# Kernel tuning notes

Measured on AMD Instinct MI355X. Metric: run time of the kernel, lower is better.

Reference implementation:

```python
import jax, jax.numpy as jnp
import numpy as np

PI = 3.141592653589793
DIM = 512          # entity/relation dim
HID = 2048         # MLP hidden dim
NREL = 500         # number of relations
NBASE = 30         # number of relation bases
B = 1024           # batch
EMB_RANGE = 0.0275 # (gamma+eps)/dim, ConE convention
AXIS_SCALE = 1.0
ARG_SCALE = 1.0
LN_EPS = 1e-5


def _ln(x):
    # LayerNorm, elementwise_affine=False
    m = x.mean(-1, keepdims=True)
    v = ((x - m) ** 2).mean(-1, keepdims=True)
    return (x - m) / jnp.sqrt(v + LN_EPS)


def _to_axis(x):
    return jnp.tanh(x) * PI


def _to_arg(x):
    return jnp.tanh(2 * x) * (PI / 2) + PI / 2


def _angle_scale(x, scale):
    return x / EMB_RANGE * scale


def setup_inputs() -> dict:
    key = jax.random.key(0)
    ks = jax.random.split(key, 16)
    D2 = 2 * DIM
    inp = {
        "source_embedding_axis": jax.random.normal(ks[0], (B, DIM), jnp.float32),
        "source_embedding_arg": jax.random.normal(ks[1], (B, DIM), jnp.float32),
        "rel_indices": jax.random.randint(ks[2], (B,), 0, NREL, jnp.int64)
        if jax.config.jax_enable_x64
        else jax.random.randint(ks[2], (B,), 0, NREL, jnp.int32),
        # rtrans branch params
        "rel_base": jax.random.normal(ks[3], (NBASE, D2, D2), jnp.float32) / np.sqrt(D2),
        "rel_att": jax.random.normal(ks[4], (NREL, NBASE), jnp.float32) * 0.05,
        "rel_bias": jax.random.normal(ks[5], (NBASE, D2), jnp.float32) * 0.05,
        # mlp branch params
        "rel_axis_embedding": jax.random.uniform(ks[6], (NREL, DIM), jnp.float32, -EMB_RANGE, EMB_RANGE),
        "rel_arg_embedding": jax.random.uniform(ks[7], (NREL, DIM), jnp.float32, -EMB_RANGE, EMB_RANGE),
        "W1": jax.random.normal(ks[8], (HID, D2), jnp.float32) * 0.02,
        "b1": jnp.zeros((HID,), jnp.float32),
        "W2": jax.random.normal(ks[9], (HID, HID), jnp.float32) * 0.02,
        "b2": jnp.zeros((HID,), jnp.float32),
        "W0": jax.random.normal(ks[10], (D2, HID), jnp.float32) * 0.02,
        "b0": jnp.zeros((D2,), jnp.float32),
        # attention fusion params
        "Wa1": jax.random.normal(ks[11], (DIM, D2), jnp.float32) * 0.02,
        "ba1": jnp.zeros((DIM,), jnp.float32),
        "Wa2": jax.random.normal(ks[12], (D2, DIM), jnp.float32) * 0.02,
        "ba2": jnp.zeros((D2,), jnp.float32),
    }
    return inp


def reference(source_embedding_axis, source_embedding_arg, rel_indices,
              rel_base, rel_att, rel_bias,
              rel_axis_embedding, rel_arg_embedding,
              W1, b1, W2, b2, W0, b0, Wa1, ba1, Wa2, ba2):
    # ---- rtrans branch ----
    att = rel_att[rel_indices]                          # (B, NBASE)
    att = _to_axis(_angle_scale(att, ARG_SCALE))        # tanh * pi
    e = jnp.concatenate([source_embedding_axis, source_embedding_arg], axis=-1)  # (B, 2D)
    # original: project_r = einsum('br,rio->bio'); out = einsum('bio,bi->bo')
    # reassociated (same math, avoids (B,2D,2D) intermediate):
    tmp = jnp.einsum('bi,rio->bro', e, rel_base)        # (B, NBASE, 2D)
    out = jnp.einsum('br,bro->bo', att, tmp)            # (B, 2D)
    bias = jnp.einsum('br,ri->bi', att, rel_bias)
    x_rtrans = _ln(out + bias)                          # (B, 2D)

    # ---- mlp branch ----
    r_axis = _to_axis(_angle_scale(rel_axis_embedding[rel_indices], AXIS_SCALE))
    r_arg = _to_arg(_angle_scale(rel_arg_embedding[rel_indices], ARG_SCALE))
    h = jnp.concatenate([source_embedding_axis + r_axis,
                         source_embedding_arg + r_arg], axis=-1)   # (B, 2D)
    h = jax.nn.relu(h @ W1.T + b1)
    h = jax.nn.relu(h @ W2.T + b2)
    x_mlp = _ln(h @ W0.T + b0)                          # (B, 2D)

    # ---- attention fusion (att_mode == 'stack') ----
    x_att = jnp.stack([x_rtrans, x_mlp])                # (2, B, 2D)
    a = jax.nn.relu(x_att @ Wa1.T + ba1)                # (2, B, D)
    attention = jax.nn.softmax(a @ Wa2.T + ba2, axis=0) # softmax over the 2 branches
    x_merged = jnp.sum(attention * x_att, axis=0)       # (B, 2D)

    axis, arg = jnp.split(x_merged, 2, axis=-1)
    return _to_axis(axis), _to_arg(arg)
```

## Files before the change

kernel.cpp:

```cpp
#include <hip/hip_runtime.h>
#include <hip/hip_bf16.h>
#include <stdint.h>

#define PI_F 3.14159265358979f
#define EMBR 0.0275f
#define BATCH 1024
#define DIM 512
#define D2 1024
#define HID 2048
#define NB 30
#define K1 (NB * D2)
#define NZ 8

using short8 = __attribute__((ext_vector_type(8))) short;
using f32x4  = __attribute__((ext_vector_type(4))) float;

#define WAITVM(N) __builtin_amdgcn_s_waitcnt(((N) & 0xF) | (((N) >> 4) << 14) | (0x7 << 4) | (0xF << 8))

__device__ __forceinline__ ushort f2bf(float f) {
  uint32_t u = __builtin_bit_cast(uint32_t, f);
  u += 0x7fffu + ((u >> 16) & 1u);
  return (ushort)(u >> 16);
}

__device__ __forceinline__ void gld_lds16(const void* g, void* l) {
  __builtin_amdgcn_global_load_lds(
      (const __attribute__((address_space(1))) uint32_t*)(uintptr_t)g,
      (__attribute__((address_space(3))) uint32_t*)(uintptr_t)l, 16, 0, 0);
}

#define TR_BLKS 7680
#define PREP_BLKS 1024
#define W1F4 (HID * D2 / 4)
#define W2F4 (HID * HID / 4)
#define W0F4 (D2 * HID / 4)
#define WA1F4 (DIM * D2 / 4)
#define WA2F4 (D2 * DIM / 4)
#define CVT_BLKS ((W1F4 + W2F4 + W0F4 + WA1F4 + WA2F4) / 256)

__global__ __launch_bounds__(256) void mega_prep(
    const float* __restrict__ rel_base, ushort* __restrict__ RBt,
    const float* __restrict__ axis, const float* __restrict__ argp,
    const int* __restrict__ rel, const float* __restrict__ rel_att,
    const float* __restrict__ rel_ax, const float* __restrict__ rel_ar,
    float* __restrict__ attb, ushort* __restrict__ Ebf, ushort* __restrict__ h0,
    const float* __restrict__ W1, const float* __restrict__ W2,
    const float* __restrict__ W0, const float* __restrict__ Wa1,
    const float* __restrict__ Wa2,
    ushort* __restrict__ W1b, ushort* __restrict__ W2b, ushort* __restrict__ W0b,
    ushort* __restrict__ Wa1b, ushort* __restrict__ Wa2b) {
  __shared__ ushort ts[64][68];
  const int bid = blockIdx.x, t = threadIdx.x;
  if (bid < TR_BLKS) {
    const int c0 = (bid & 15) * 64, r0 = (bid >> 4) * 64;
    const int tc = (t & 15) * 4;
    const int tr = t >> 4;
#pragma unroll
    for (int j = 0; j < 4; ++j) {
      const int r = tr + j * 16;
      float4 v = *(const float4*)&rel_base[(size_t)(r0 + r) * D2 + c0 + tc];
      ushort4 o;
      o.x = f2bf(v.x); o.y = f2bf(v.y); o.z = f2bf(v.z); o.w = f2bf(v.w);
      *(ushort4*)&ts[r][tc] = o;
    }
    __syncthreads();
#pragma unroll
    for (int j = 0; j < 4; ++j) {
      const int c = tr + j * 16;
      ushort4 v;
      v.x = ts[tc + 0][c]; v.y = ts[tc + 1][c];
      v.z = ts[tc + 2][c]; v.w = ts[tc + 3][c];
      *(ushort4*)&RBt[(size_t)(c0 + c) * K1 + r0 + tc] = v;
    }
  } else if (bid < TR_BLKS + PREP_BLKS) {
    const int b = bid - TR_BLKS;
    const int ri = rel[b];
    if (t < NB)
      attb[b * 32 + t] = tanhf(rel_att[ri * NB + t] * (1.f / EMBR)) * PI_F;
    for (int i = t; i < DIM; i += 256) {
      const float ax = axis[(size_t)b * DIM + i];
      const float ag = argp[(size_t)b * DIM + i];
      Ebf[(size_t)b * D2 + i]       = f2bf(ax);
      Ebf[(size_t)b * D2 + DIM + i] = f2bf(ag);
      const float ra = rel_ax[(size_t)ri * DIM + i];
      const float rg = rel_ar[(size_t)ri * DIM + i];
      h0[(size_t)b * D2 + i] = f2bf(ax + tanhf(ra * (1.f / EMBR)) * PI_F);
      h0[(size_t)b * D2 + DIM + i] =
          f2bf(ag + tanhf(2.f * rg * (1.f / EMBR)) * (PI_F * 0.5f) + PI_F * 0.5f);
    }
  } else {
    int i = (bid - TR_BLKS - PREP_BLKS) * 256 + t;
    const float* s; ushort* d;
    if (i < W1F4) { s = W1; d = W1b; }
    else if ((i -= W1F4) < W2F4) { s = W2; d = W2b; }
    else if ((i -= W2F4) < W0F4) { s = W0; d = W0b; }
    else if ((i -= W0F4) < WA1F4) { s = Wa1; d = Wa1b; }
    else { i -= WA1F4; s = Wa2; d = Wa2b; }
    float4 v = ((const float4*)s)[i];
    ushort4 o;
    o.x = f2bf(v.x); o.y = f2bf(v.y); o.z = f2bf(v.z); o.w = f2bf(v.w);
    ((ushort4*)d)[i] = o;
  }
}

template <int EPI>
__global__ __launch_bounds__(256, 2) void gemm_nt(
    const ushort* __restrict__ A, const ushort* __restrict__ Bt,
    const float* __restrict__ bias, float* __restrict__ Cf,
    ushort* __restrict__ Cb, int M, int N, int K) {
  __shared__ ushort As[4][128 * 32];
  __shared__ ushort Bs[4][128 * 32];
  const int tid  = threadIdx.x;
  const int lane = tid & 63, wave = tid >> 6;
  const int wm = wave >> 1, wn = wave & 1;
  const int lrow = lane & 15, quad = lane >> 4;
  const int m0 = blockIdx.y * 128, n0 = blockIdx.x * 128;
  const int T = K >> 5;

  const int rr = lane >> 2;
  const int eo = (lane & 3) * 8;
  const int c1 = wave, c2 = wave + 4;
  const ushort* Ag1 = A  + (size_t)(m0 + c1 * 16 + rr) * K + eo;
  const ushort* Ag2 = A  + (size_t)(m0 + c2 * 16 + rr) * K + eo;
  const ushort* Bg1 = Bt + (size_t)(n0 + c1 * 16 + rr) * K + eo;
  const ushort* Bg2 = Bt + (size_t)(n0 + c2 * 16 + rr) * K + eo;

  auto issue = [&](int slot) {
    const int t  = (slot < T - 1) ? slot : T - 1;
    const int bf = slot & 3;
    const int kk = t << 5;
    gld_lds16(Ag1 + kk, &As[bf][c1 * 512]);
    gld_lds16(Ag2 + kk, &As[bf][c2 * 512]);
    gld_lds16(Bg1 + kk, &Bs[bf][c1 * 512]);
    gld_lds16(Bg2 + kk, &Bs[bf][c2 * 512]);
  };

  f32x4 acc[4][4] = {};
  issue(0); issue(1); issue(2);

  for (int t = 0; t < T; ++t) {
    WAITVM(8);
    __builtin_amdgcn_s_barrier();
    issue(t + 3);
    const ushort* as = As[t & 3];
    const ushort* bs = Bs[t & 3];
    short8 af[4], bq[4];
#pragma unroll
    for (int i = 0; i < 4; ++i) {
      af[i] = *(const short8*)&as[(wm * 64 + i * 16 + lrow) * 32 + quad * 8];
      bq[i] = *(const short8*)&bs[(wn * 64 + i * 16 + lrow) * 32 + quad * 8];
    }
#pragma unroll
    for (int mi = 0; mi < 4; ++mi)
#pragma unroll
      for (int ni = 0; ni < 4; ++ni)
        acc[mi][ni] = __builtin_amdgcn_mfma_f32_16x16x32_bf16(
            af[mi], bq[ni], acc[mi][ni], 0, 0, 0);
  }
  WAITVM(0);

  const int colBase = n0 + wn * 64;
  const int rowBase = m0 + wm * 64;
#pragma unroll
  for (int mi = 0; mi < 4; ++mi) {
#pragma unroll
    for (int ni = 0; ni < 4; ++ni) {
      const int col  = colBase + ni * 16 + lrow;
      const int row0 = rowBase + mi * 16 + quad * 4;
      const float bv = bias[col];
      if (EPI == 1) {
#pragma unroll
        for (int g = 0; g < 4; ++g)
          Cb[(size_t)(row0 + g) * N + col] = f2bf(fmaxf(acc[mi][ni][g] + bv, 0.f));
      } else {
#pragma unroll
        for (int g = 0; g < 4; ++g)
          Cf[(size_t)(row0 + g) * N + col] = acc[mi][ni][g] + bv;
      }
    }
  }
}

__global__ __launch_bounds__(256, 2) void gemm_rtrans(
    const ushort* __restrict__ E, const ushort* __restrict__ RBt,
    const float* __restrict__ attb, float* __restrict__ C1p) {
  __shared__ ushort As[4][128 * 32];
  __shared__ ushort Bs[4][128 * 32];
  __shared__ float attS[4 * 128];
  const int tid  = threadIdx.x;
  const int lane = tid & 63, wave = tid >> 6;
  const int wm = wave >> 1, wn = wave & 1;
  const int lrow = lane & 15, quad = lane >> 4;
  const int m0 = blockIdx.y * 128, n0 = blockIdx.x * 128;
  const int z = blockIdx.z;
  const int r_start = (z < 7) ? z * 4 : 27;
  const int r_cnt   = (z < 6) ? 4 : 3;
  const int T = r_cnt << 5;

  for (int idx = tid; idx < r_cnt * 128; idx += 256)
    attS[idx] = attb[(size_t)(m0 + (idx & 127)) * 32 + r_start + (idx >> 7)];

  const int rr = lane >> 2;
  const int eo = (lane & 3) * 8;
  const int c1 = wave, c2 = wave + 4;
  const ushort* Ag1 = E + (size_t)(m0 + c1 * 16 + rr) * D2 + eo;
  const ushort* Ag2 = E + (size_t)(m0 + c2 * 16 + rr) * D2 + eo;
  const ushort* Bg1 = RBt + (size_t)(n0 + c1 * 16 + rr) * K1 + eo;
  const ushort* Bg2 = RBt + (size_t)(n0 + c2 * 16 + rr) * K1 + eo;

  auto issue = [&](int slot) {
    const int t  = (slot < T - 1) ? slot : T - 1;
    const int bf = slot & 3;
    const int ka = (t & 31) << 5;
    const size_t kb = ((size_t)(r_start + (t >> 5)) << 10) + ka;
    gld_lds16(Ag1 + ka, &As[bf][c1 * 512]);
    gld_lds16(Ag2 + ka, &As[bf][c2 * 512]);
    gld_lds16(Bg1 + kb, &Bs[bf][c1 * 512]);
    gld_lds16(Bg2 + kb, &Bs[bf][c2 * 512]);
  };

  f32x4 acc[4][4] = {};
  f32x4 acc2[4][4] = {};
  issue(0); issue(1); issue(2);
  __syncthreads();

  for (int t = 0; t < T; ++t) {
    WAITVM(8);
    __builtin_amdgcn_s_barrier();
    issue(t + 3);
    const ushort* as = As[t & 3];
    const ushort* bs = Bs[t & 3];
    short8 af[4], bq[4];
#pragma unroll
    for (int i = 0; i < 4; ++i) {
      af[i] = *(const short8*)&as[(wm * 64 + i * 16 + lrow) * 32 + quad * 8];
      bq[i] = *(const short8*)&bs[(wn * 64 + i * 16 + lrow) * 32 + quad * 8];
    }
#pragma unroll
    for (int mi = 0; mi < 4; ++mi)
#pragma unroll
      for (int ni = 0; ni < 4; ++ni)
        acc[mi][ni] = __builtin_amdgcn_mfma_f32_16x16x32_bf16(
            af[mi], bq[ni], acc[mi][ni], 0, 0, 0);
    if ((t & 31) == 31) {
      const int rl = t >> 5;
#pragma unroll
      for (int mi = 0; mi < 4; ++mi)
#pragma unroll
        for (int g = 0; g < 4; ++g) {
          const float s = attS[rl * 128 + wm * 64 + mi * 16 + quad * 4 + g];
#pragma unroll
          for (int ni = 0; ni < 4; ++ni) {
            acc2[mi][ni][g] += s * acc[mi][ni][g];
            acc[mi][ni][g] = 0.f;
          }
        }
    }
  }
  WAITVM(0);

  float* dst = C1p + (size_t)z * BATCH * D2;
  const int colBase = n0 + wn * 64;
  const int rowBase = m0 + wm * 64;
#pragma unroll
  for (int mi = 0; mi < 4; ++mi)
#pragma unroll
    for (int ni = 0; ni < 4; ++ni) {
      const int col  = colBase + ni * 16 + lrow;
      const int row0 = rowBase + mi * 16 + quad * 4;
#pragma unroll
      for (int g = 0; g < 4; ++g)
        dst[(size_t)(row0 + g) * D2 + col] = acc2[mi][ni][g];
    }
}

__global__ __launch_bounds__(256) void reduce_ln_rt(
    const float* __restrict__ C1p, const float* __restrict__ att,
    const float* __restrict__ rel_bias, float* __restrict__ xf,
    ushort* __restrict__ Xb) {
  const int b = blockIdx.x, t = threadIdx.x;
  __shared__ float attS[NB];
  __shared__ float sa[4], sb[4];
  if (t < NB) attS[t] = att[b * 32 + t];
  __syncthreads();
  float v[4], sum = 0.f, sq = 0.f;
#pragma unroll
  for (int j = 0; j < 4; ++j) {
    const int o = j * 256 + t;
    float acc = 0.f;
#pragma unroll
    for (int s = 0; s < NZ; ++s)
      acc += C1p[((size_t)s * BATCH + b) * D2 + o];
    float bias = 0.f;
    for (int r = 0; r < NB; ++r) bias += attS[r] * rel_bias[r * D2 + o];
    acc += bias;
    v[j] = acc; sum += acc; sq += acc * acc;
  }
  const int lane = t & 63, wv = t >> 6;
  for (int off = 32; off > 0; off >>= 1) {
    sum += __shfl_down(sum, off, 64);
    sq  += __shfl_down(sq, off, 64);
  }
  if (lane == 0) { sa[wv] = sum; sb[wv] = sq; }
  __syncthreads();
  const float S = sa[0] + sa[1] + sa[2] + sa[3];
  const float Q = sb[0] + sb[1] + sb[2] + sb[3];
  const float mean = S / D2;
  const float inv = rsqrtf(fmaxf(Q / D2 - mean * mean, 0.f) + 1e-5f);
#pragma unroll
  for (int j = 0; j < 4; ++j) {
    const int o = j * 256 + t;
    const float y = (v[j] - mean) * inv;
    xf[(size_t)b * D2 + o] = y;
    Xb[(size_t)b * D2 + o] = f2bf(y);
  }
}

__global__ __launch_bounds__(256) void ln_rows(
    const float* __restrict__ G, float* __restrict__ xf, ushort* __restrict__ Xb) {
  const int b = blockIdx.x, t = threadIdx.x;
  __shared__ float sa[4], sb[4];
  float v[4], sum = 0.f, sq = 0.f;
#pragma unroll
  for (int j = 0; j < 4; ++j) {
    const int o = j * 256 + t;
    v[j] = G[(size_t)b * D2 + o];
    sum += v[j]; sq += v[j] * v[j];
  }
  const int lane = t & 63, wv = t >> 6;
  for (int off = 32; off > 0; off >>= 1) {
    sum += __shfl_down(sum, off, 64);
    sq  += __shfl_down(sq, off, 64);
  }
  if (lane == 0) { sa[wv] = sum; sb[wv] = sq; }
  __syncthreads();
  const float S = sa[0] + sa[1] + sa[2] + sa[3];
  const float Q = sb[0] + sb[1] + sb[2] + sb[3];
  const float mean = S / D2;
  const float inv = rsqrtf(fmaxf(Q / D2 - mean * mean, 0.f) + 1e-5f);
#pragma unroll
  for (int j = 0; j < 4; ++j) {
    const int o = j * 256 + t;
    const float y = (v[j] - mean) * inv;
    xf[(size_t)b * D2 + o] = y;
    Xb[(size_t)b * D2 + o] = f2bf(y);
  }
}

__global__ __launch_bounds__(256) void fuse_out(
    const float* __restrict__ L, const float* __restrict__ xrt,
    const float* __restrict__ xml, float* __restrict__ out) {
  const int b = blockIdx.x, t = threadIdx.x;
#pragma unroll
  for (int j = 0; j < 4; ++j) {
    const int o = j * 256 + t;
    const float l0 = L[(size_t)b * D2 + o];
    const float l1 = L[(size_t)(BATCH + b) * D2 + o];
    const float w0 = 1.f / (1.f + expf(l1 - l0));
    const float m = w0 * xrt[(size_t)b * D2 + o] +
                    (1.f - w0) * xml[(size_t)b * D2 + o];
    if (o < DIM)
      out[(size_t)b * DIM + o] = tanhf(m) * PI_F;
    else
      out[(size_t)BATCH * DIM + (size_t)b * DIM + (o - DIM)] =
          tanhf(2.f * m) * (PI_F * 0.5f) + PI_F * 0.5f;
  }
}

extern "C" void kernel_launch(void* const* d_in, const int* in_sizes, int n_in,
                              void* d_out, int out_size, void* d_ws, size_t ws_size,
                              hipStream_t stream) {
  (void)in_sizes; (void)n_in; (void)out_size; (void)ws_size;
  const float* s_axis   = (const float*)d_in[0];
  const float* s_arg    = (const float*)d_in[1];
  const int*   rel      = (const int*)d_in[2];
  const float* rel_base = (const float*)d_in[3];
  const float* rel_att  = (const float*)d_in[4];
  const float* rel_bias = (const float*)d_in[5];
  const float* rel_ax_e = (const float*)d_in[6];
  const float* rel_ar_e = (const float*)d_in[7];
  const float* W1 = (const float*)d_in[8];
  const float* b1 = (const float*)d_in[9];
  const float* W2 = (const float*)d_in[10];
  const float* b2 = (const float*)d_in[11];
  const float* W0 = (const float*)d_in[12];
  const float* b0 = (const float*)d_in[13];
  const float* Wa1 = (const float*)d_in[14];
  const float* ba1 = (const float*)d_in[15];
  const float* Wa2 = (const float*)d_in[16];
  const float* ba2 = (const float*)d_in[17];

  char* ws = (char*)d_ws;
  size_t off = 0;
  ushort* RBt  = (ushort*)(ws + off); off += (size_t)K1 * D2 * 2;
  float*  C1p  = (float*)(ws + off);  off += (size_t)NZ * BATCH * D2 * 4;
  ushort* Ebf  = (ushort*)(ws + off); off += (size_t)BATCH * D2 * 2;
  ushort* W1b  = (ushort*)(ws + off); off += (size_t)HID * D2 * 2;
  ushort* W2b  = (ushort*)(ws + off); off += (size_t)HID * HID * 2;
  ushort* W0b  = (ushort*)(ws + off); off += (size_t)D2 * HID * 2;
  ushort* Wa1b = (ushort*)(ws + off); off += (size_t)DIM * D2 * 2;
  ushort* Wa2b = (ushort*)(ws + off); off += (size_t)D2 * DIM * 2;
  ushort* h0   = (ushort*)(ws + off); off += (size_t)BATCH * D2 * 2;
  ushort* Xb   = (ushort*)(ws + off); off += (size_t)2 * BATCH * D2 * 2;
  float*  xrt  = (float*)(ws + off);  off += (size_t)BATCH * D2 * 4;
  float*  xml  = (float*)(ws + off);  off += (size_t)BATCH * D2 * 4;
  float*  attb = (float*)(ws + off);  off += (size_t)BATCH * 32 * 4;
  char* ali = (char*)C1p;
  ushort* H1  = (ushort*)ali; ali += (size_t)BATCH * HID * 2;
  ushort* H2  = (ushort*)ali; ali += (size_t)BATCH * HID * 2;
  float*  G0  = (float*)ali;  ali += (size_t)BATCH * D2 * 4;
  ushort* Aat = (ushort*)ali; ali += (size_t)2 * BATCH * DIM * 2;
  float*  Lg  = (float*)ali;  ali += (size_t)2 * BATCH * D2 * 4;

  mega_prep<<<TR_BLKS + PREP_BLKS + CVT_BLKS, 256, 0, stream>>>(
      rel_base, RBt, s_axis, s_arg, rel, rel_att, rel_ax_e, rel_ar_e,
      attb, Ebf, h0, W1, W2, W0, Wa1, Wa2, W1b, W2b, W0b, Wa1b, Wa2b);
  gemm_rtrans<<<dim3(D2 / 128, BATCH / 128, NZ), 256, 0, stream>>>(
      Ebf, RBt, attb, C1p);
  reduce_ln_rt<<<BATCH, 256, 0, stream>>>(C1p, attb, rel_bias, xrt, Xb);
  gemm_nt<1><<<dim3(HID / 128, BATCH / 128), 256, 0, stream>>>(
      h0, W1b, b1, nullptr, H1, BATCH, HID, D2);
  gemm_nt<1><<<dim3(HID / 128, BATCH / 128), 256, 0, stream>>>(
      H1, W2b, b2, nullptr, H2, BATCH, HID, HID);
  gemm_nt<2><<<dim3(D2 / 128, BATCH / 128), 256, 0, stream>>>(
      H2, W0b, b0, G0, nullptr, BATCH, D2, HID);
  ln_rows<<<BATCH, 256, 0, stream>>>(G0, xml, Xb + (size_t)BATCH * D2);
  gemm_nt<1><<<dim3(DIM / 128, 2 * BATCH / 128), 256, 0, stream>>>(
      Xb, Wa1b, ba1, nullptr, Aat, 2 * BATCH, DIM, D2);
  gemm_nt<2><<<dim3(D2 / 128, 2 * BATCH / 128), 256, 0, stream>>>(
      Aat, Wa2b, ba2, Lg, nullptr, 2 * BATCH, D2, DIM);
  fuse_out<<<BATCH, 256, 0, stream>>>(Lg, xrt, xml, (float*)d_out);
}
```

Before: 433.2 us.

## Split-K all GEMMs with separate reduce kernels and per-basis rtrans partials

```diff
diff --git a/kernel.cpp b/kernel.cpp
--- a/kernel.cpp
+++ b/kernel.cpp
@@ -10,13 +10,15 @@
 #define HID 2048
 #define NB 30
 #define K1 (NB * D2)
-#define NZ 8
 
 using short8 = __attribute__((ext_vector_type(8))) short;
 using f32x4  = __attribute__((ext_vector_type(4))) float;
 
 #define WAITVM(N) __builtin_amdgcn_s_waitcnt(((N) & 0xF) | (((N) >> 4) << 14) | (0x7 << 4) | (0xF << 8))
 
+__device__ __forceinline__ float bf2f(ushort u) {
+  union { uint32_t i; float f; } v; v.i = ((uint32_t)u) << 16; return v.f;
+}
 __device__ __forceinline__ ushort f2bf(float f) {
   uint32_t u = __builtin_bit_cast(uint32_t, f);
   u += 0x7fffu + ((u >> 16) & 1u);
@@ -103,32 +105,31 @@
   }
 }
 
-template <int EPI>
-__global__ __launch_bounds__(256, 2) void gemm_nt(
+__global__ __launch_bounds__(256, 3) void gemm_nt(
     const ushort* __restrict__ A, const ushort* __restrict__ Bt,
-    const float* __restrict__ bias, float* __restrict__ Cf,
-    ushort* __restrict__ Cb, int M, int N, int K) {
-  __shared__ ushort As[4][128 * 32];
-  __shared__ ushort Bs[4][128 * 32];
+    float* __restrict__ Cf, int M, int N, int K, int kLen) {
+  __shared__ ushort As[3][128 * 32];
+  __shared__ ushort Bs[3][128 * 32];
   const int tid  = threadIdx.x;
   const int lane = tid & 63, wave = tid >> 6;
   const int wm = wave >> 1, wn = wave & 1;
   const int lrow = lane & 15, quad = lane >> 4;
   const int m0 = blockIdx.y * 128, n0 = blockIdx.x * 128;
-  const int T = K >> 5;
+  const int kStart = blockIdx.z * kLen;
+  const int T = kLen >> 5;
 
   const int rr = lane >> 2;
   const int eo = (lane & 3) * 8;
   const int c1 = wave, c2 = wave + 4;
-  const ushort* Ag1 = A  + (size_t)(m0 + c1 * 16 + rr) * K + eo;
-  const ushort* Ag2 = A  + (size_t)(m0 + c2 * 16 + rr) * K + eo;
-  const ushort* Bg1 = Bt + (size_t)(n0 + c1 * 16 + rr) * K + eo;
-  const ushort* Bg2 = Bt + (size_t)(n0 + c2 * 16 + rr) * K + eo;
+  const ushort* Ag1 = A  + (size_t)(m0 + c1 * 16 + rr) * K + kStart + eo;
+  const ushort* Ag2 = A  + (size_t)(m0 + c2 * 16 + rr) * K + kStart + eo;
+  const ushort* Bg1 = Bt + (size_t)(n0 + c1 * 16 + rr) * K + kStart + eo;
+  const ushort* Bg2 = Bt + (size_t)(n0 + c2 * 16 + rr) * K + kStart + eo;
 
   auto issue = [&](int slot) {
-    const int t  = (slot < T - 1) ? slot : T - 1;
-    const int bf = slot & 3;
-    const int kk = t << 5;
+    const int tt = (slot < T - 1) ? slot : T - 1;
+    const int bf = slot % 3;
+    const int kk = tt << 5;
     gld_lds16(Ag1 + kk, &As[bf][c1 * 512]);
     gld_lds16(Ag2 + kk, &As[bf][c2 * 512]);
     gld_lds16(Bg1 + kk, &Bs[bf][c1 * 512]);
@@ -136,14 +137,14 @@
   };
 
   f32x4 acc[4][4] = {};
-  issue(0); issue(1); issue(2);
+  issue(0); issue(1);
 
   for (int t = 0; t < T; ++t) {
-    WAITVM(8);
+    WAITVM(4);
     __builtin_amdgcn_s_barrier();
-    issue(t + 3);
-    const ushort* as = As[t & 3];
-    const ushort* bs = Bs[t & 3];
+    issue(t + 2);
+    const ushort* as = As[t % 3];
+    const ushort* bs = Bs[t % 3];
     short8 af[4], bq[4];
 #pragma unroll
     for (int i = 0; i < 4; ++i) {
@@ -159,77 +160,65 @@
   }
   WAITVM(0);
 
+  float* dst = Cf + (size_t)blockIdx.z * M * N;
   const int colBase = n0 + wn * 64;
   const int rowBase = m0 + wm * 64;
 #pragma unroll
-  for (int mi = 0; mi < 4; ++mi) {
+  for (int mi = 0; mi < 4; ++mi)
 #pragma unroll
     for (int ni = 0; ni < 4; ++ni) {
       const int col  = colBase + ni * 16 + lrow;
       const int row0 = rowBase + mi * 16 + quad * 4;
-      const float bv = bias[col];
-      if (EPI == 1) {
-#pragma unroll
-        for (int g = 0; g < 4; ++g)
-          Cb[(size_t)(row0 + g) * N + col] = f2bf(fmaxf(acc[mi][ni][g] + bv, 0.f));
-      } else {
-#pragma unroll
-        for (int g = 0; g < 4; ++g)
-          Cf[(size_t)(row0 + g) * N + col] = acc[mi][ni][g] + bv;
-      }
-    }
-  }
-}
-
-__global__ __launch_bounds__(256, 2) void gemm_rtrans(
+#pragma unroll
+      for (int g = 0; g < 4; ++g)
+        dst[(size_t)(row0 + g) * N + col] = acc[mi][ni][g];
+    }
+}
+
+__global__ __launch_bounds__(256, 3) void gemm_rtrans(
     const ushort* __restrict__ E, const ushort* __restrict__ RBt,
-    const float* __restrict__ attb, float* __restrict__ C1p) {
-  __shared__ ushort As[4][128 * 32];
-  __shared__ ushort Bs[4][128 * 32];
-  __shared__ float attS[4 * 128];
+    const float* __restrict__ attb, ushort* __restrict__ Pb) {
+  __shared__ ushort As[3][128 * 32];
+  __shared__ ushort Bs[3][128 * 32];
+  __shared__ float attS[128];
   const int tid  = threadIdx.x;
   const int lane = tid & 63, wave = tid >> 6;
   const int wm = wave >> 1, wn = wave & 1;
   const int lrow = lane & 15, quad = lane >> 4;
   const int m0 = blockIdx.y * 128, n0 = blockIdx.x * 128;
   const int z = blockIdx.z;
-  const int r_start = (z < 7) ? z * 4 : 27;
-  const int r_cnt   = (z < 6) ? 4 : 3;
-  const int T = r_cnt << 5;
-
-  for (int idx = tid; idx < r_cnt * 128; idx += 256)
-    attS[idx] = attb[(size_t)(m0 + (idx & 127)) * 32 + r_start + (idx >> 7)];
+  const int T = 32;
+
+  if (tid < 128) attS[tid] = attb[(size_t)(m0 + tid) * 32 + z];
+  __syncthreads();
 
   const int rr = lane >> 2;
   const int eo = (lane & 3) * 8;
   const int c1 = wave, c2 = wave + 4;
   const ushort* Ag1 = E + (size_t)(m0 + c1 * 16 + rr) * D2 + eo;
   const ushort* Ag2 = E + (size_t)(m0 + c2 * 16 + rr) * D2 + eo;
-  const ushort* Bg1 = RBt + (size_t)(n0 + c1 * 16 + rr) * K1 + eo;
-  const ushort* Bg2 = RBt + (size_t)(n0 + c2 * 16 + rr) * K1 + eo;
+  const ushort* Bg1 = RBt + (size_t)(n0 + c1 * 16 + rr) * K1 + ((size_t)z << 10) + eo;
+  const ushort* Bg2 = RBt + (size_t)(n0 + c2 * 16 + rr) * K1 + ((size_t)z << 10) + eo;
 
   auto issue = [&](int slot) {
-    const int t  = (slot < T - 1) ? slot : T - 1;
-    const int bf = slot & 3;
-    const int ka = (t & 31) << 5;
-    const size_t kb = ((size_t)(r_start + (t >> 5)) << 10) + ka;
-    gld_lds16(Ag1 + ka, &As[bf][c1 * 512]);
-    gld_lds16(Ag2 + ka, &As[bf][c2 * 512]);
-    gld_lds16(Bg1 + kb, &Bs[bf][c1 * 512]);
-    gld_lds16(Bg2 + kb, &Bs[bf][c2 * 512]);
+    const int tt = (slot < T - 1) ? slot : T - 1;
+    const int bf = slot % 3;
+    const int kk = tt << 5;
+    gld_lds16(Ag1 + kk, &As[bf][c1 * 512]);
+    gld_lds16(Ag2 + kk, &As[bf][c2 * 512]);
+    gld_lds16(Bg1 + kk, &Bs[bf][c1 * 512]);
+    gld_lds16(Bg2 + kk, &Bs[bf][c2 * 512]);
   };
 
   f32x4 acc[4][4] = {};
-  f32x4 acc2[4][4] = {};
-  issue(0); issue(1); issue(2);
-  __syncthreads();
+  issue(0); issue(1);
 
   for (int t = 0; t < T; ++t) {
-    WAITVM(8);
+    WAITVM(4);
     __builtin_amdgcn_s_barrier();
-    issue(t + 3);
-    const ushort* as = As[t & 3];
-    const ushort* bs = Bs[t & 3];
+    issue(t + 2);
+    const ushort* as = As[t % 3];
+    const ushort* bs = Bs[t % 3];
     short8 af[4], bq[4];
 #pragma unroll
     for (int i = 0; i < 4; ++i) {
@@ -242,24 +231,10 @@
       for (int ni = 0; ni < 4; ++ni)
         acc[mi][ni] = __builtin_amdgcn_mfma_f32_16x16x32_bf16(
             af[mi], bq[ni], acc[mi][ni], 0, 0, 0);
-    if ((t & 31) == 31) {
-      const int rl = t >> 5;
-#pragma unroll
-      for (int mi = 0; mi < 4; ++mi)
-#pragma unroll
-        for (int g = 0; g < 4; ++g) {
-          const float s = attS[rl * 128 + wm * 64 + mi * 16 + quad * 4 + g];
-#pragma unroll
-          for (int ni = 0; ni < 4; ++ni) {
-            acc2[mi][ni][g] += s * acc[mi][ni][g];
-            acc[mi][ni][g] = 0.f;
-          }
-        }
-    }
   }
   WAITVM(0);
 
-  float* dst = C1p + (size_t)z * BATCH * D2;
+  ushort* dst = Pb + (size_t)z * BATCH * D2;
   const int colBase = n0 + wn * 64;
   const int rowBase = m0 + wm * 64;
 #pragma unroll
@@ -269,13 +244,15 @@
       const int col  = colBase + ni * 16 + lrow;
       const int row0 = rowBase + mi * 16 + quad * 4;
 #pragma unroll
-      for (int g = 0; g < 4; ++g)
-        dst[(size_t)(row0 + g) * D2 + col] = acc2[mi][ni][g];
+      for (int g = 0; g < 4; ++g) {
+        const float s = attS[wm * 64 + mi * 16 + quad * 4 + g];
+        dst[(size_t)(row0 + g) * D2 + col] = f2bf(s * acc[mi][ni][g]);
+      }
     }
 }
 
 __global__ __launch_bounds__(256) void reduce_ln_rt(
-    const float* __restrict__ C1p, const float* __restrict__ att,
+    const ushort* __restrict__ Pb, const float* __restrict__ att,
     const float* __restrict__ rel_bias, float* __restrict__ xf,
     ushort* __restrict__ Xb) {
   const int b = blockIdx.x, t = threadIdx.x;
@@ -283,19 +260,21 @@
   __shared__ float sa[4], sb[4];
   if (t < NB) attS[t] = att[b * 32 + t];
   __syncthreads();
-  float v[4], sum = 0.f, sq = 0.f;
-#pragma unroll
-  for (int j = 0; j < 4; ++j) {
-    const int o = j * 256 + t;
-    float acc = 0.f;
-#pragma unroll
-    for (int s = 0; s < NZ; ++s)
-      acc += C1p[((size_t)s * BATCH + b) * D2 + o];
-    float bias = 0.f;
-    for (int r = 0; r < NB; ++r) bias += attS[r] * rel_bias[r * D2 + o];
-    acc += bias;
-    v[j] = acc; sum += acc; sq += acc * acc;
-  }
+  const int o0 = t * 4;
+  float v[4] = {};
+#pragma unroll
+  for (int r = 0; r < NB; ++r) {
+    ushort4 p = *(const ushort4*)&Pb[((size_t)r * BATCH + b) * D2 + o0];
+    v[0] += bf2f(p.x); v[1] += bf2f(p.y); v[2] += bf2f(p.z); v[3] += bf2f(p.w);
+  }
+#pragma unroll
+  for (int r = 0; r < NB; ++r) {
+    const float a = attS[r];
+    float4 rb = *(const float4*)&rel_bias[(size_t)r * D2 + o0];
+    v[0] += a * rb.x; v[1] += a * rb.y; v[2] += a * rb.z; v[3] += a * rb.w;
+  }
+  float sum = v[0] + v[1] + v[2] + v[3];
+  float sq  = v[0]*v[0] + v[1]*v[1] + v[2]*v[2] + v[3]*v[3];
   const int lane = t & 63, wv = t >> 6;
   for (int off = 32; off > 0; off >>= 1) {
     sum += __shfl_down(sum, off, 64);
@@ -307,26 +286,50 @@
   const float Q = sb[0] + sb[1] + sb[2] + sb[3];
   const float mean = S / D2;
   const float inv = rsqrtf(fmaxf(Q / D2 - mean * mean, 0.f) + 1e-5f);
-#pragma unroll
-  for (int j = 0; j < 4; ++j) {
-    const int o = j * 256 + t;
-    const float y = (v[j] - mean) * inv;
-    xf[(size_t)b * D2 + o] = y;
-    Xb[(size_t)b * D2 + o] = f2bf(y);
-  }
+  float4 yo; ushort4 yb;
+  yo.x = (v[0] - mean) * inv; yb.x = f2bf(yo.x);
+  yo.y = (v[1] - mean) * inv; yb.y = f2bf(yo.y);
+  yo.z = (v[2] - mean) * inv; yb.z = f2bf(yo.z);
+  yo.w = (v[3] - mean) * inv; yb.w = f2bf(yo.w);
+  *(float4*)&xf[(size_t)b * D2 + o0] = yo;
+  *(ushort4*)&Xb[(size_t)b * D2 + o0] = yb;
+}
+
+__global__ __launch_bounds__(256) void reduce_relu_bf16(
+    const float* __restrict__ P, const float* __restrict__ bias,
+    ushort* __restrict__ out, int S, int MN, int N) {
+  const int i = blockIdx.x * 256 + threadIdx.x;
+  const int e0 = i * 4;
+  if (e0 >= MN) return;
+  float4 a = ((const float4*)P)[i];
+  for (int s = 1; s < S; ++s) {
+    float4 p = *(const float4*)&P[(size_t)s * MN + e0];
+    a.x += p.x; a.y += p.y; a.z += p.z; a.w += p.w;
+  }
+  float4 bv = *(const float4*)&bias[e0 & (N - 1)];
+  ushort4 o;
+  o.x = f2bf(fmaxf(a.x + bv.x, 0.f));
+  o.y = f2bf(fmaxf(a.y + bv.y, 0.f));
+  o.z = f2bf(fmaxf(a.z + bv.z, 0.f));
+  o.w = f2bf(fmaxf(a.w + bv.w, 0.f));
+  ((ushort4*)out)[i] = o;
 }
 
 __global__ __launch_bounds__(256) void ln_rows(
-    const float* __restrict__ G, float* __restrict__ xf, ushort* __restrict__ Xb) {
+    const float* __restrict__ P, const float* __restrict__ b0, int S,
+    float* __restrict__ xf, ushort* __restrict__ Xb) {
   const int b = blockIdx.x, t = threadIdx.x;
   __shared__ float sa[4], sb[4];
-  float v[4], sum = 0.f, sq = 0.f;
-#pragma unroll
-  for (int j = 0; j < 4; ++j) {
-    const int o = j * 256 + t;
-    v[j] = G[(size_t)b * D2 + o];
-    sum += v[j]; sq += v[j] * v[j];
-  }
+  const int o0 = t * 4;
+  float4 a = *(const float4*)&P[(size_t)b * D2 + o0];
+  for (int s = 1; s < S; ++s) {
+    float4 p = *(const float4*)&P[(size_t)s * BATCH * D2 + (size_t)b * D2 + o0];
+    a.x += p.x; a.y += p.y; a.z += p.z; a.w += p.w;
+  }
+  float4 bv = *(const float4*)&b0[o0];
+  float v[4] = {a.x + bv.x, a.y + bv.y, a.z + bv.z, a.w + bv.w};
+  float sum = v[0] + v[1] + v[2] + v[3];
+  float sq  = v[0]*v[0] + v[1]*v[1] + v[2]*v[2] + v[3]*v[3];
   const int lane = t & 63, wv = t >> 6;
   for (int off = 32; off > 0; off >>= 1) {
     sum += __shfl_down(sum, off, 64);
@@ -334,37 +337,50 @@
   }
   if (lane == 0) { sa[wv] = sum; sb[wv] = sq; }
   __syncthreads();
-  const float S = sa[0] + sa[1] + sa[2] + sa[3];
-  const float Q = sb[0] + sb[1] + sb[2] + sb[3];
-  const float mean = S / D2;
+  const float S_ = sa[0] + sa[1] + sa[2] + sa[3];
+  const float Q  = sb[0] + sb[1] + sb[2] + sb[3];
+  const float mean = S_ / D2;
   const float inv = rsqrtf(fmaxf(Q / D2 - mean * mean, 0.f) + 1e-5f);
+  float4 yo; ushort4 yb;
+  yo.x = (v[0] - mean) * inv; yb.x = f2bf(yo.x);
+  yo.y = (v[1] - mean) * inv; yb.y = f2bf(yo.y);
+  yo.z = (v[2] - mean) * inv; yb.z = f2bf(yo.z);
+  yo.w = (v[3] - mean) * inv; yb.w = f2bf(yo.w);
+  *(float4*)&xf[(size_t)b * D2 + o0] = yo;
+  *(ushort4*)&Xb[(size_t)b * D2 + o0] = yb;
+}
+
+__global__ __launch_bounds__(256) void fuse_out(
+    const float* __restrict__ P, const float* __restrict__ ba2, int S,
+    const float* __restrict__ xrt, const float* __restrict__ xml,
+    float* __restrict__ out) {
+  const int b = blockIdx.x, t = threadIdx.x;
+  const int o0 = t * 4;
+  float4 l0 = *(const float4*)&P[(size_t)b * D2 + o0];
+  float4 l1 = *(const float4*)&P[(size_t)(BATCH + b) * D2 + o0];
+  for (int s = 1; s < S; ++s) {
+    const float* Ps = P + (size_t)s * 2 * BATCH * D2;
+    float4 p0 = *(const float4*)&Ps[(size_t)b * D2 + o0];
+    float4 p1 = *(const float4*)&Ps[(size_t)(BATCH + b) * D2 + o0];
+    l0.x += p0.x; l0.y += p0.y; l0.z += p0.z; l0.w += p0.w;
+    l1.x += p1.x; l1.y += p1.y; l1.z += p1.z; l1.w += p1.w;
+  }
+  float4 xr = *(const float4*)&xrt[(size_t)b * D2 + o0];
+  float4 xm = *(const float4*)&xml[(size_t)b * D2 + o0];
+  float r[4];
 #pragma unroll
   for (int j = 0; j < 4; ++j) {
-    const int o = j * 256 + t;
-    const float y = (v[j] - mean) * inv;
-    xf[(size_t)b * D2 + o] = y;
-    Xb[(size_t)b * D2 + o] = f2bf(y);
-  }
-}
-
-__global__ __launch_bounds__(256) void fuse_out(
-    const float* __restrict__ L, const float* __restrict__ xrt,
-    const float* __restrict__ xml, float* __restrict__ out) {
-  const int b = blockIdx.x, t = threadIdx.x;
-#pragma unroll
-  for (int j = 0; j < 4; ++j) {
-    const int o = j * 256 + t;
-    const float l0 = L[(size_t)b * D2 + o];
-    const float l1 = L[(size_t)(BATCH + b) * D2 + o];
-    const float w0 = 1.f / (1.f + expf(l1 - l0));
-    const float m = w0 * xrt[(size_t)b * D2 + o] +
-                    (1.f - w0) * xml[(size_t)b * D2 + o];
-    if (o < DIM)
-      out[(size_t)b * DIM + o] = tanhf(m) * PI_F;
-    else
-      out[(size_t)BATCH * DIM + (size_t)b * DIM + (o - DIM)] =
-          tanhf(2.f * m) * (PI_F * 0.5f) + PI_F * 0.5f;
-  }
+    const float a0 = ((const float*)&l0)[j];
+    const float a1 = ((const float*)&l1)[j];
+    const float w0 = 1.f / (1.f + expf(a1 - a0));
+    const float m = w0 * ((const float*)&xr)[j] + (1.f - w0) * ((const float*)&xm)[j];
+    r[j] = (o0 < DIM) ? tanhf(m) * PI_F
+                      : tanhf(2.f * m) * (PI_F * 0.5f) + PI_F * 0.5f;
+  }
+  float* dst = (o0 < DIM)
+      ? &out[(size_t)b * DIM + o0]
+      : &out[(size_t)BATCH * DIM + (size_t)b * DIM + (o0 - DIM)];
+  *(float4*)dst = {r[0], r[1], r[2], r[3]};
 }
 
 extern "C" void kernel_launch(void* const* d_in, const int* in_sizes, int n_in,
@@ -393,7 +409,9 @@
   char* ws = (char*)d_ws;
   size_t off = 0;
   ushort* RBt  = (ushort*)(ws + off); off += (size_t)K1 * D2 * 2;
-  float*  C1p  = (float*)(ws + off);  off += (size_t)NZ * BATCH * D2 * 4;
+  char*   Pzone= ws + off;            off += (size_t)NB * BATCH * D2 * 2;
+  ushort* Pb   = (ushort*)Pzone;
+  float*  P    = (float*)Pzone;
   ushort* Ebf  = (ushort*)(ws + off); off += (size_t)BATCH * D2 * 2;
   ushort* W1b  = (ushort*)(ws + off); off += (size_t)HID * D2 * 2;
   ushort* W2b  = (ushort*)(ws + off); off += (size_t)HID * HID * 2;
@@ -402,32 +420,38 @@
   ushort* Wa2b = (ushort*)(ws + off); off += (size_t)D2 * DIM * 2;
   ushort* h0   = (ushort*)(ws + off); off += (size_t)BATCH * D2 * 2;
   ushort* Xb   = (ushort*)(ws + off); off += (size_t)2 * BATCH * D2 * 2;
+  ushort* H1   = (ushort*)(ws + off); off += (size_t)BATCH * HID * 2;
+  ushort* H2   = (ushort*)(ws + off); off += (size_t)BATCH * HID * 2;
+  ushort* Aat  = (ushort*)(ws + off); off += (size_t)2 * BATCH * DIM * 2;
   float*  xrt  = (float*)(ws + off);  off += (size_t)BATCH * D2 * 4;
   float*  xml  = (float*)(ws + off);  off += (size_t)BATCH * D2 * 4;
   float*  attb = (float*)(ws + off);  off += (size_t)BATCH * 32 * 4;
-  char* ali = (char*)C1p;
-  ushort* H1  = (ushort*)ali; ali += (size_t)BATCH * HID * 2;
-  ushort* H2  = (ushort*)ali; ali += (size_t)BATCH * HID * 2;
-  float*  G0  = (float*)ali;  ali += (size_t)BATCH * D2 * 4;
-  ushort* Aat = (ushort*)ali; ali += (size_t)2 * BATCH * DIM * 2;
-  float*  Lg  = (float*)ali;  ali += (size_t)2 * BATCH * D2 * 4;
 
   mega_prep<<<TR_BLKS + PREP_BLKS + CVT_BLKS, 256, 0, stream>>>(
       rel_base, RBt, s_axis, s_arg, rel, rel_att, rel_ax_e, rel_ar_e,
       attb, Ebf, h0, W1, W2, W0, Wa1, Wa2, W1b, W2b, W0b, Wa1b, Wa2b);
-  gemm_rtrans<<<dim3(D2 / 128, BATCH / 128, NZ), 256, 0, stream>>>(
-      Ebf, RBt, attb, C1p);
-  reduce_ln_rt<<<BATCH, 256, 0, stream>>>(C1p, attb, rel_bias, xrt, Xb);
-  gemm_nt<1><<<dim3(HID / 128, BATCH / 128), 256, 0, stream>>>(
-      h0, W1b, b1, nullptr, H1, BATCH, HID, D2);
-  gemm_nt<1><<<dim3(HID / 128, BATCH / 128), 256, 0, stream>>>(
-      H1, W2b, b2, nullptr, H2, BATCH, HID, HID);
-  gemm_nt<2><<<dim3(D2 / 128, BATCH / 128), 256, 0, stream>>>(
-      H2, W0b, b0, G0, nullptr, BATCH, D2, HID);
-  ln_rows<<<BATCH, 256, 0, stream>>>(G0, xml, Xb + (size_t)BATCH * D2);
-  gemm_nt<1><<<dim3(DIM / 128, 2 * BATCH / 128), 256, 0, stream>>>(
-      Xb, Wa1b, ba1, nullptr, Aat, 2 * BATCH, DIM, D2);
-  gemm_nt<2><<<dim3(D2 / 128, 2 * BATCH / 128), 256, 0, stream>>>(
-      Aat, Wa2b, ba2, Lg, nullptr, 2 * BATCH, D2, DIM);
-  fuse_out<<<BATCH, 256, 0, stream>>>(Lg, xrt, xml, (float*)d_out);
-}
+
+  gemm_rtrans<<<dim3(D2 / 128, BATCH / 128, NB), 256, 0, stream>>>(
+      Ebf, RBt, attb, Pb);
+  reduce_ln_rt<<<BATCH, 256, 0, stream>>>(Pb, attb, rel_bias, xrt, Xb);
+
+  gemm_nt<<<dim3(HID / 128, BATCH / 128, 4), 256, 0, stream>>>(
+      h0, W1b, P, BATCH, HID, D2, D2 / 4);
+  reduce_relu_bf16<<<BATCH * HID / 1024, 256, 0, stream>>>(
+      P, b1, H1, 4, BATCH * HID, HID);
+  gemm_nt<<<dim3(HID / 128, BATCH / 128, 4), 256, 0, stream>>>(
+      H1, W2b, P, BATCH, HID, HID, HID / 4);
+  reduce_relu_bf16<<<BATCH * HID / 1024, 256, 0, stream>>>(
+      P, b2, H2, 4, BATCH * HID, HID);
+  gemm_nt<<<dim3(D2 / 128, BATCH / 128, 8), 256, 0, stream>>>(
+      H2, W0b, P, BATCH, D2, HID, HID / 8);
+  ln_rows<<<BATCH, 256, 0, stream>>>(P, b0, 8, xml, Xb + (size_t)BATCH * D2);
+
+  gemm_nt<<<dim3(DIM / 128, 2 * BATCH / 128, 8), 256, 0, stream>>>(
+      Xb, Wa1b, P, 2 * BATCH, DIM, D2, D2 / 8);
+  reduce_relu_bf16<<<2 * BATCH * DIM / 1024, 256, 0, stream>>>(
+      P, ba1, Aat, 8, 2 * BATCH * DIM, DIM);
+  gemm_nt<<<dim3(D2 / 128, 2 * BATCH / 128, 4), 256, 0, stream>>>(
+      Aat, Wa2b, P, 2 * BATCH, D2, DIM, DIM / 4);
+  fuse_out<<<BATCH, 256, 0, stream>>>(P, ba2, 4, xrt, xml, (float*)d_out);
+}
```

Measured after the change: 455.4 us. +5.1%, slower.
